# Kernel optimization log

Measured on AMD Instinct MI355X. Metric: run time of the kernel, lower is better.

The kernel has to match this reference:

```python
import math
import jax, jax.numpy as jnp
import numpy as np

B, N, D = 16, 2304, 1024
H = W = 1344
M = 8
HV = WV = 48  # h_vis = h_patches//2; N == HV*WV
N_RAYS, N_SAMPLES = 24, 20
K_STEEP, THETA = 50.0, 0.3


def setup_inputs() -> dict:
    key = jax.random.key(0)
    ks = jax.random.split(key, 6)
    visual_tokens = jax.random.normal(ks[0], (B, N, D), jnp.float32)
    depth_map = jax.random.uniform(ks[1], (B, H, W), jnp.float32) * 10.0
    masks = jax.random.randint(ks[2], (M, H, W), 0, 2).astype(jnp.int32)
    rgb_gate_w = jax.random.normal(ks[3], (D,), jnp.float32) / math.sqrt(D)
    depth_w = jax.random.normal(ks[4], (28, D), jnp.float32) / math.sqrt(28.0)
    depth_b = jnp.zeros((D,), jnp.float32)
    ln_gamma = jnp.ones((D,), jnp.float32)
    ln_beta = jnp.zeros((D,), jnp.float32)
    return dict(visual_tokens=visual_tokens, depth_map=depth_map, masks=masks,
                rgb_gate_w=rgb_gate_w, depth_w=depth_w, depth_b=depth_b,
                ln_gamma=ln_gamma, ln_beta=ln_beta, h_vis=HV, w_vis=WV)


def _bilinear_border(img, x, y):
    # img [B,H,W]; x,y [P] pixel coords; F.grid_sample bilinear, border pad, align_corners=True
    Hh, Ww = img.shape[-2], img.shape[-1]
    x = jnp.clip(x, 0.0, Ww - 1.0)
    y = jnp.clip(y, 0.0, Hh - 1.0)
    x0 = jnp.floor(x); y0 = jnp.floor(y)
    wx = x - x0; wy = y - y0
    x0i = x0.astype(jnp.int32); y0i = y0.astype(jnp.int32)
    x1i = jnp.minimum(x0i + 1, Ww - 1); y1i = jnp.minimum(y0i + 1, Hh - 1)
    v00 = img[:, y0i, x0i]; v01 = img[:, y0i, x1i]
    v10 = img[:, y1i, x0i]; v11 = img[:, y1i, x1i]
    return v00 * (1 - wx) * (1 - wy) + v01 * wx * (1 - wy) + v10 * (1 - wx) * wy + v11 * wx * wy


def _bilinear_zeros(img, x, y):
    # img [H,W]; F.grid_sample bilinear, zeros pad, align_corners=True
    Hh, Ww = img.shape
    x0 = jnp.floor(x); y0 = jnp.floor(y)
    wx = x - x0; wy = y - y0
    x0i = x0.astype(jnp.int32); y0i = y0.astype(jnp.int32)
    x1i = x0i + 1; y1i = y0i + 1

    def tap(yy, xx, w):
        valid = (xx >= 0) & (xx < Ww) & (yy >= 0) & (yy < Hh)
        v = img[jnp.clip(yy, 0, Hh - 1), jnp.clip(xx, 0, Ww - 1)]
        return jnp.where(valid, v * w, 0.0)

    return (tap(y0i, x0i, (1 - wx) * (1 - wy)) + tap(y0i, x1i, wx * (1 - wy)) +
            tap(y1i, x0i, (1 - wx) * wy) + tap(y1i, x1i, wx * wy))


def _forward(visual_tokens, depth_map, masks, rgb_gate_w, depth_w, depth_b, ln_gamma, ln_beta, h_vis, w_vis):
    Bn, Hh, Ww = depth_map.shape
    ph, pw = Hh // h_vis, Ww // w_vis  # adaptive_avg_pool2d divides evenly -> block mean
    angles = jnp.linspace(0.0, 2.0 * math.pi, N_RAYS + 1)[:-1]
    cos_a, sin_a = jnp.cos(angles), jnp.sin(angles)
    max_r = min(Hh, Ww) * 0.45
    t_vals = jnp.linspace(0.0, max_r, N_SAMPLES)

    def per_mask(binm_i):
        binm = binm_i.astype(jnp.float32)  # [H,W] binary (RLE-decoded in torch)
        coverage = binm.reshape(h_vis, ph, w_vis, pw).mean(axis=(1, 3))  # [hv,wv]
        soft2d = jax.nn.sigmoid(K_STEEP * (coverage - THETA))
        # --- DB-style soft gated attention pool over N tokens ---
        log_soft = jnp.log(jnp.clip(soft2d.reshape(-1), 1e-8))
        scores = jnp.einsum('bnd,d->bn', visual_tokens, rgb_gate_w)
        weights = jax.nn.softmax(scores + log_soft[None, :], axis=-1)
        rgb = jnp.einsum('bn,bnd->bd', weights, visual_tokens)
        # --- masked depth stats (mean, unbiased std) ---
        count = binm.sum()
        mean_d = jnp.einsum('bhw,hw->b', depth_map, binm) / jnp.maximum(count, 1.0)
        sq = jnp.einsum('bhw,hw->b', depth_map * depth_map, binm)
        var = (sq - count * mean_d * mean_d) / jnp.maximum(count - 1.0, 1.0)
        std_d = jnp.sqrt(jnp.clip(jnp.where(count > 1.0, var, 0.0), 0.0))
        # --- soft centroid (normalized to ~[0,1]) ---
        soft_sum = soft2d.sum() + 1e-8
        cx = (soft2d.sum(0) * jnp.arange(w_vis, dtype=jnp.float32)).sum() / (soft_sum * w_vis)
        cy = (soft2d.sum(1) * jnp.arange(h_vis, dtype=jnp.float32)).sum() / (soft_sum * h_vis)
        # --- 24-ray radial depth profile ---
        cx_pix = cx * (Ww - 1); cy_pix = cy * (Hh - 1)
        xs_pix = cx_pix + cos_a[:, None] * t_vals[None, :]  # [rays,samples]
        ys_pix = cy_pix + sin_a[:, None] * t_vals[None, :]
        d_samp = _bilinear_border(depth_map, xs_pix.ravel(), ys_pix.ravel()).reshape(Bn, N_RAYS, N_SAMPLES)
        xs_p = xs_pix / (Ww - 1) * (w_vis - 1)
        ys_p = ys_pix / (Hh - 1) * (h_vis - 1)
        sw = _bilinear_zeros(soft2d, xs_p.ravel(), ys_p.ravel()).reshape(N_RAYS, N_SAMPLES)
        sw = jnp.clip(sw, 1e-6)
        w_norm = sw / sw.sum(axis=1, keepdims=True)
        profile = (d_samp * w_norm[None]).sum(-1)  # [B,rays]
        stats = jnp.concatenate([mean_d[:, None], std_d[:, None],
                                 jnp.broadcast_to(cx, (Bn, 1)), jnp.broadcast_to(cy, (Bn, 1)),
                                 profile], axis=1)  # [B,28]
        stats = jnp.where(count > 0.0, stats, 0.0)  # empty-mask fallback
        # --- depth_proj: Linear(28->D) + LayerNorm ---
        h = stats @ depth_w + depth_b
        mu = h.mean(-1, keepdims=True)
        v = ((h - mu) ** 2).mean(-1, keepdims=True)
        dep = (h - mu) / jnp.sqrt(v + 1e-5) * ln_gamma + ln_beta
        return rgb, dep

    return jax.vmap(per_mask)(masks)  # ([M,B,D], [M,B,D])


def reference(visual_tokens, depth_map, masks, rgb_gate_w, depth_w, depth_b, ln_gamma, ln_beta, h_vis, w_vis):
    return _forward(visual_tokens, depth_map, masks, rgb_gate_w, depth_w, depth_b,
                    ln_gamma, ln_beta, int(h_vis), int(w_vis))
```

## Files before the change

### kernel.cpp

```cpp
#include <hip/hip_runtime.h>
#include <math.h>

constexpr int BN   = 16;
constexpr int NTOK = 2304;
constexpr int DDIM = 1024;
constexpr int HH   = 1344;
constexpr int WWp  = 1344;
constexpr int HWPIX = HH * WWp;
constexpr int NM   = 8;
constexpr int HVIS = 48;
constexpr int PATCH = 28;
constexpr int NRAY = 24;
constexpr int NSMP = 20;
constexpr int NPROB = HVIS * HVIS;

__global__ void k_pack(const int* __restrict__ masks, uchar4* __restrict__ packed,
                       float* __restrict__ cnt, float* __restrict__ sumd,
                       float* __restrict__ sumd2) {
    int i = blockIdx.x * blockDim.x + threadIdx.x;
    if (blockIdx.x == 0) {
        int t = threadIdx.x;
        if (t < 8) cnt[t] = 0.f;
        else if (t < 136) sumd[t - 8] = 0.f;
        else if (t < 264) sumd2[t - 136] = 0.f;
    }
    unsigned b0 = 0, b1 = 0, b2 = 0, b3 = 0;
#pragma unroll
    for (int m = 0; m < 8; m++) {
        int4 mv = ((const int4*)(masks + (size_t)m * HWPIX))[i];
        b0 |= (unsigned)(mv.x & 1) << m;
        b1 |= (unsigned)(mv.y & 1) << m;
        b2 |= (unsigned)(mv.z & 1) << m;
        b3 |= (unsigned)(mv.w & 1) << m;
    }
    packed[i] = make_uchar4((unsigned char)b0, (unsigned char)b1,
                            (unsigned char)b2, (unsigned char)b3);
}

__global__ void k_cov(const unsigned char* __restrict__ packed,
                      float* __restrict__ cov, float* __restrict__ cnt) {
    int patch = blockIdx.x;
    int pi = patch / HVIS, pj = patch - pi * HVIS;
    int t = threadIdx.x;
    float c[8] = {0, 0, 0, 0, 0, 0, 0, 0};
    for (int p = t; p < PATCH * PATCH; p += 256) {
        int r = p / PATCH, q = p - r * PATCH;
        unsigned pb = packed[(pi * PATCH + r) * WWp + pj * PATCH + q];
#pragma unroll
        for (int m = 0; m < 8; m++) c[m] += (float)((pb >> m) & 1u);
    }
    __shared__ float red[8][256];
#pragma unroll
    for (int m = 0; m < 8; m++) red[m][t] = c[m];
    __syncthreads();
    for (int o = 128; o; o >>= 1) {
        if (t < o) {
#pragma unroll
            for (int m = 0; m < 8; m++) red[m][t] += red[m][t + o];
        }
        __syncthreads();
    }
    if (t < 8) {
        cov[t * NPROB + patch] = red[t][0];
        atomicAdd(&cnt[t], red[t][0]);
    }
}

__global__ void k_scores(const float* __restrict__ tokens,
                         const float* __restrict__ gate,
                         float* __restrict__ scores) {
    int row = blockIdx.x * 4 + (threadIdx.x >> 6);
    int lane = threadIdx.x & 63;
    const float4* tp = (const float4*)(tokens + (size_t)row * DDIM);
    const float4* gp = (const float4*)gate;
    float s = 0.f;
#pragma unroll
    for (int i = 0; i < 4; i++) {
        int idx = lane + i * 64;
        float4 tv = tp[idx];
        float4 gv = gp[idx];
        s += tv.x * gv.x + tv.y * gv.y + tv.z * gv.z + tv.w * gv.w;
    }
#pragma unroll
    for (int o = 32; o; o >>= 1) s += __shfl_down(s, o, 64);
    if (lane == 0) scores[row] = s;
}

__global__ void k_soft(const float* __restrict__ cov, float* __restrict__ soft,
                       float* __restrict__ lsoft, float* __restrict__ cent) {
    int m = blockIdx.x, t = threadIdx.x;
    float psum = 0.f, psx = 0.f, psy = 0.f;
#pragma unroll
    for (int i = 0; i < 9; i++) {
        int n = t + i * 256;
        float c = cov[m * NPROB + n] * (1.0f / 784.0f);
        float s = 1.0f / (1.0f + expf(-50.0f * (c - 0.3f)));
        soft[m * NPROB + n] = s;
        lsoft[m * NPROB + n] = logf(fmaxf(s, 1e-8f));
        int row = n / HVIS, col = n - row * HVIS;
        psum += s;
        psx += s * (float)col;
        psy += s * (float)row;
    }
    __shared__ float r0[256], r1[256], r2[256];
    r0[t] = psum; r1[t] = psx; r2[t] = psy;
    __syncthreads();
    for (int o = 128; o; o >>= 1) {
        if (t < o) { r0[t] += r0[t + o]; r1[t] += r1[t + o]; r2[t] += r2[t + o]; }
        __syncthreads();
    }
    if (t == 0) {
        float ss = r0[0] + 1e-8f;
        float cx = r1[0] / (ss * (float)HVIS);
        float cy = r2[0] / (ss * (float)HVIS);
        cent[m * 4 + 0] = cx;
        cent[m * 4 + 1] = cy;
        cent[m * 4 + 2] = cx * (float)(WWp - 1);
        cent[m * 4 + 3] = cy * (float)(HH - 1);
    }
}

constexpr int KPT = 7;
__global__ void k_depthstats(const float* __restrict__ depth,
                             const uchar4* __restrict__ packed,
                             float* __restrict__ sumd, float* __restrict__ sumd2) {
    int b = blockIdx.y;
    int t = threadIdx.x;
    int base4 = blockIdx.x * (256 * KPT);
    const float4* dp4 = (const float4*)(depth + (size_t)b * HWPIX);

    float4 dv[KPT];
    uchar4 pv[KPT];
#pragma unroll
    for (int k = 0; k < KPT; k++) {
        int idx = base4 + k * 256 + t;
        dv[k] = dp4[idx];
        pv[k] = packed[idx];
    }

    float acc[8] = {0, 0, 0, 0, 0, 0, 0, 0};
    float acc2[8] = {0, 0, 0, 0, 0, 0, 0, 0};
#pragma unroll
    for (int k = 0; k < KPT; k++) {
        float dd[4] = {dv[k].x, dv[k].y, dv[k].z, dv[k].w};
        unsigned bb[4] = {pv[k].x, pv[k].y, pv[k].z, pv[k].w};
#pragma unroll
        for (int j = 0; j < 4; j++) {
            float d = dd[j];
            float sq = d * d;
            unsigned byte = bb[j];
#pragma unroll
            for (int m = 0; m < 8; m++) {
                float f = (float)((byte >> m) & 1u);
                acc[m] = fmaf(f, d, acc[m]);
                acc2[m] = fmaf(f, sq, acc2[m]);
            }
        }
    }
#pragma unroll
    for (int o = 32; o; o >>= 1) {
#pragma unroll
        for (int m = 0; m < 8; m++) {
            acc[m] += __shfl_down(acc[m], o, 64);
            acc2[m] += __shfl_down(acc2[m], o, 64);
        }
    }
    __shared__ float red[2][8][4];
    int wid = threadIdx.x >> 6, lane = threadIdx.x & 63;
    if (lane == 0) {
#pragma unroll
        for (int m = 0; m < 8; m++) {
            red[0][m][wid] = acc[m];
            red[1][m][wid] = acc2[m];
        }
    }
    __syncthreads();
    if (threadIdx.x < 16) {
        int s = threadIdx.x >> 3, m = threadIdx.x & 7;
        float v = red[s][m][0] + red[s][m][1] + red[s][m][2] + red[s][m][3];
        atomicAdd((s ? sumd2 : sumd) + m * BN + b, v);
    }
}

__global__ void k_rays(const float* __restrict__ depth, const float* __restrict__ soft,
                       const float* __restrict__ cent, float* __restrict__ prof) {
    int m = blockIdx.x, b = blockIdx.y, t = threadIdx.x;
    __shared__ float s_sw[NRAY * NSMP], s_d[NRAY * NSMP];
    float cxp = cent[m * 4 + 2], cyp = cent[m * 4 + 3];
    if (t < NRAY * NSMP) {
        int r = t / NSMP, s = t - r * NSMP;
        float ang = (float)r * (6.28318530717958647692f / (float)NRAY);
        float tv = (float)s * (604.8f / (float)(NSMP - 1));
        float xs = fmaf(cosf(ang), tv, cxp);
        float ys = fmaf(sinf(ang), tv, cyp);
        float x = fminf(fmaxf(xs, 0.0f), (float)(WWp - 1));
        float y = fminf(fmaxf(ys, 0.0f), (float)(HH - 1));
        float x0f = floorf(x), y0f = floorf(y);
        float wx = x - x0f, wy = y - y0f;
        int x0 = (int)x0f, y0 = (int)y0f;
        int x1 = min(x0 + 1, WWp - 1), y1 = min(y0 + 1, HH - 1);
        const float* dpb = depth + (size_t)b * HWPIX;
        float v00 = dpb[y0 * WWp + x0], v01 = dpb[y0 * WWp + x1];
        float v10 = dpb[y1 * WWp + x0], v11 = dpb[y1 * WWp + x1];
        float ds = v00 * (1 - wx) * (1 - wy) + v01 * wx * (1 - wy) +
                   v10 * (1 - wx) * wy + v11 * wx * wy;
        const float* sp = soft + m * NPROB;
        float xp = xs * ((float)(HVIS - 1) / (float)(WWp - 1));
        float yp = ys * ((float)(HVIS - 1) / (float)(HH - 1));
        float xp0 = floorf(xp), yp0 = floorf(yp);
        float ux = xp - xp0, uy = yp - yp0;
        int a0 = (int)xp0, c0 = (int)yp0;
        float sw = 0.f;
        int xx[2] = {a0, a0 + 1};
        int yy[2] = {c0, c0 + 1};
        float wxt[2] = {1.0f - ux, ux};
        float wyt[2] = {1.0f - uy, uy};
#pragma unroll
        for (int ii = 0; ii < 2; ii++) {
#pragma unroll
            for (int jj = 0; jj < 2; jj++) {
                int yv = yy[ii], xv = xx[jj];
                bool valid = (xv >= 0) && (xv < HVIS) && (yv >= 0) && (yv < HVIS);
                float vv = sp[min(max(yv, 0), HVIS - 1) * HVIS + min(max(xv, 0), HVIS - 1)];
                sw += valid ? vv * wyt[ii] * wxt[jj] : 0.0f;
            }
        }
        sw = fmaxf(sw, 1e-6f);
        s_sw[t] = sw;
        s_d[t] = ds;
    }
    __syncthreads();
    if (t < NRAY) {
        float wsum = 0.f, dot = 0.f;
#pragma unroll
        for (int s = 0; s < NSMP; s++) {
            float w = s_sw[t * NSMP + s];
            wsum += w;
            dot += s_d[t * NSMP + s] * w;
        }
        prof[(m * BN + b) * NRAY + t] = dot / wsum;
    }
}

__global__ void k_wred(const float* __restrict__ scores, const float* __restrict__ lsoft,
                       float* __restrict__ smax, float* __restrict__ ssum) {
    int mb = blockIdx.x;
    int m = mb >> 4, b = mb & 15;
    int t = threadIdx.x;
    float v[9];
    float pm = -1e30f;
#pragma unroll
    for (int i = 0; i < 9; i++) {
        int n = t + i * 256;
        float x = scores[b * NTOK + n] + lsoft[m * NTOK + n];
        v[i] = x;
        pm = fmaxf(pm, x);
    }
    __shared__ float r[256];
    r[t] = pm;
    __syncthreads();
    for (int o = 128; o; o >>= 1) {
        if (t < o) r[t] = fmaxf(r[t], r[t + o]);
        __syncthreads();
    }
    float mx = r[0];
    __syncthreads();
    float ps = 0.f;
#pragma unroll
    for (int i = 0; i < 9; i++) ps += expf(v[i] - mx);
    r[t] = ps;
    __syncthreads();
    for (int o = 128; o; o >>= 1) {
        if (t < o) r[t] += r[t + o];
        __syncthreads();
    }
    if (t == 0) { smax[mb] = mx; ssum[mb] = r[0]; }
}

__global__ void k_rgb(const float* __restrict__ tokens, const float* __restrict__ scores,
                      const float* __restrict__ lsoft, const float* __restrict__ smax,
                      const float* __restrict__ ssum, float* __restrict__ rgb) {
    constexpr int CHUNK = 72;
    int b = blockIdx.x, chunk = blockIdx.y, t = threadIdx.x;
    int n0 = chunk * CHUNK;
    __shared__ float wl[8][CHUNK];
    for (int i = t; i < 8 * CHUNK; i += 256) {
        int m = i / CHUNK, k = i - m * CHUNK;
        int n = n0 + k;
        wl[m][k] = expf(scores[b * NTOK + n] + lsoft[m * NTOK + n] - smax[m * BN + b]) /
                   ssum[m * BN + b];
    }
    __syncthreads();
    float acc[8][4] = {};
    const float4* tp = (const float4*)(tokens + ((size_t)(b * NTOK + n0)) * DDIM);
#pragma unroll 8
    for (int k = 0; k < CHUNK; k++) {
        float4 tok = tp[(size_t)k * 256 + t];
#pragma unroll
        for (int m = 0; m < 8; m++) {
            float w = wl[m][k];
            acc[m][0] = fmaf(w, tok.x, acc[m][0]);
            acc[m][1] = fmaf(w, tok.y, acc[m][1]);
            acc[m][2] = fmaf(w, tok.z, acc[m][2]);
            acc[m][3] = fmaf(w, tok.w, acc[m][3]);
        }
    }
    int d0 = t * 4;
#pragma unroll
    for (int m = 0; m < 8; m++) {
#pragma unroll
        for (int j = 0; j < 4; j++)
            atomicAdd(&rgb[((size_t)(m * BN + b)) * DDIM + d0 + j], acc[m][j]);
    }
}

__global__ void k_dep(const float* __restrict__ sumd, const float* __restrict__ sumd2,
                      const float* __restrict__ cnt, const float* __restrict__ cent,
                      const float* __restrict__ prof, const float* __restrict__ dw,
                      const float* __restrict__ db, const float* __restrict__ gamma,
                      const float* __restrict__ beta, float* __restrict__ dep) {
    int m = blockIdx.x, b = blockIdx.y, t = threadIdx.x;
    __shared__ float st[28];
    float c = cnt[m];
    if (t < 28) {
        float v;
        if (t == 0) {
            v = sumd[m * BN + b] / fmaxf(c, 1.0f);
        } else if (t == 1) {
            float mean = sumd[m * BN + b] / fmaxf(c, 1.0f);
            float var = (sumd2[m * BN + b] - c * mean * mean) / fmaxf(c - 1.0f, 1.0f);
            var = (c > 1.0f) ? var : 0.0f;
            v = sqrtf(fmaxf(var, 0.0f));
        } else if (t == 2) v = cent[m * 4 + 0];
        else if (t == 3) v = cent[m * 4 + 1];
        else v = prof[(m * BN + b) * NRAY + (t - 4)];
        st[t] = (c > 0.0f) ? v : 0.0f;
    }
    __syncthreads();
    int d0 = t * 4;
    float4 hb = *(const float4*)(db + d0);
    float h0 = hb.x, h1 = hb.y, h2 = hb.z, h3 = hb.w;
#pragma unroll
    for (int k = 0; k < 28; k++) {
        float s = st[k];
        float4 w = *(const float4*)(dw + k * DDIM + d0);
        h0 = fmaf(s, w.x, h0);
        h1 = fmaf(s, w.y, h1);
        h2 = fmaf(s, w.z, h2);
        h3 = fmaf(s, w.w, h3);
    }
    float ps = h0 + h1 + h2 + h3;
    float pq = h0 * h0 + h1 * h1 + h2 * h2 + h3 * h3;
    __shared__ float rs[256], rq[256];
    rs[t] = ps; rq[t] = pq;
    __syncthreads();
    for (int o = 128; o; o >>= 1) {
        if (t < o) { rs[t] += rs[t + o]; rq[t] += rq[t + o]; }
        __syncthreads();
    }
    float mu = rs[0] * (1.0f / (float)DDIM);
    float var = rq[0] * (1.0f / (float)DDIM) - mu * mu;
    float inv = 1.0f / sqrtf(var + 1e-5f);
    float4 g = *(const float4*)(gamma + d0);
    float4 be = *(const float4*)(beta + d0);
    size_t o = ((size_t)(m * BN + b)) * DDIM + d0;
    dep[o + 0] = (h0 - mu) * inv * g.x + be.x;
    dep[o + 1] = (h1 - mu) * inv * g.y + be.y;
    dep[o + 2] = (h2 - mu) * inv * g.z + be.z;
    dep[o + 3] = (h3 - mu) * inv * g.w + be.w;
}

extern "C" void kernel_launch(void* const* d_in, const int* in_sizes, int n_in,
                              void* d_out, int out_size, void* d_ws, size_t ws_size,
                              hipStream_t stream) {
    const float* tokens = (const float*)d_in[0];
    const float* depth  = (const float*)d_in[1];
    const int*   masks  = (const int*)d_in[2];
    const float* gate   = (const float*)d_in[3];
    const float* dw     = (const float*)d_in[4];
    const float* db     = (const float*)d_in[5];
    const float* gamma  = (const float*)d_in[6];
    const float* beta   = (const float*)d_in[7];
    float* out = (float*)d_out;

    char* ws = (char*)d_ws;
    size_t off = 0;
    auto alloc = [&](size_t bytes) {
        size_t o = off;
        off = (off + bytes + 255) & ~(size_t)255;
        return o;
    };
    unsigned char* packed = (unsigned char*)(ws + alloc(HWPIX));
    float* cov    = (float*)(ws + alloc((size_t)NM * NPROB * 4));
    float* cnt    = (float*)(ws + alloc(NM * 4));
    float* soft   = (float*)(ws + alloc((size_t)NM * NPROB * 4));
    float* lsoft  = (float*)(ws + alloc((size_t)NM * NPROB * 4));
    float* cent   = (float*)(ws + alloc(NM * 4 * 4));
    float* sumd   = (float*)(ws + alloc(NM * BN * 4));
    float* sumd2  = (float*)(ws + alloc(NM * BN * 4));
    float* scores = (float*)(ws + alloc((size_t)BN * NTOK * 4));
    float* smax   = (float*)(ws + alloc(NM * BN * 4));
    float* ssum   = (float*)(ws + alloc(NM * BN * 4));
    float* prof   = (float*)(ws + alloc((size_t)NM * BN * NRAY * 4));

    hipMemsetAsync(out, 0, (size_t)NM * BN * DDIM * 4, stream);

    k_pack<<<HWPIX / 4 / 256, 256, 0, stream>>>(masks, (uchar4*)packed,
                                                cnt, sumd, sumd2);
    k_cov<<<NPROB, 256, 0, stream>>>(packed, cov, cnt);
    k_scores<<<BN * NTOK / 4, 256, 0, stream>>>(tokens, gate, scores);
    k_soft<<<NM, 256, 0, stream>>>(cov, soft, lsoft, cent);
    k_depthstats<<<dim3(HWPIX / 4 / (256 * KPT), BN), 256, 0, stream>>>(
        depth, (const uchar4*)packed, sumd, sumd2);
    k_rays<<<dim3(NM, BN), 512, 0, stream>>>(depth, soft, cent, prof);
    k_wred<<<NM * BN, 256, 0, stream>>>(scores, lsoft, smax, ssum);
    k_rgb<<<dim3(BN, NTOK / 72), 256, 0, stream>>>(tokens, scores, lsoft, smax, ssum, out);
    k_dep<<<dim3(NM, BN), 256, 0, stream>>>(sumd, sumd2, cnt, cent, prof, dw, db,
                                            gamma, beta,
                                            out + (size_t)NM * BN * DDIM);
}
```

Measured before the change: 543.1 us.

## Batch global loads ahead of compute with sched barriers and launch bounds

Several kernels (mask packing, score dot products, depth statistics, rgb pooling) now issue all their global loads up front into registers. A scheduling barrier separates those loads from the arithmetic so more memory requests are in flight at once. Launch bounds are added, depth-stats work per thread drops from 7 to 4, and the rgb weight tile in shared memory is transposed so the 8 per-mask weights come from two vector reads. The risk is higher register pressure, and the barriers stop the compiler from interleaving loads and math on its own.

After: 621.0 us. 1.14x slower.

```diff
diff --git a/kernel.cpp b/kernel.cpp
--- a/kernel.cpp
+++ b/kernel.cpp
@@ -14,9 +14,10 @@
 constexpr int NSMP = 20;
 constexpr int NPROB = HVIS * HVIS;
 
-__global__ void k_pack(const int* __restrict__ masks, uchar4* __restrict__ packed,
-                       float* __restrict__ cnt, float* __restrict__ sumd,
-                       float* __restrict__ sumd2) {
+__global__ __launch_bounds__(256, 4) void k_pack(
+        const int* __restrict__ masks, uchar4* __restrict__ packed,
+        float* __restrict__ cnt, float* __restrict__ sumd,
+        float* __restrict__ sumd2) {
     int i = blockIdx.x * blockDim.x + threadIdx.x;
     if (blockIdx.x == 0) {
         int t = threadIdx.x;
@@ -24,14 +25,18 @@
         else if (t < 136) sumd[t - 8] = 0.f;
         else if (t < 264) sumd2[t - 136] = 0.f;
     }
+    int4 mv[8];
+#pragma unroll
+    for (int m = 0; m < 8; m++)
+        mv[m] = ((const int4*)(masks + (size_t)m * HWPIX))[i];
+    __builtin_amdgcn_sched_barrier(0);
     unsigned b0 = 0, b1 = 0, b2 = 0, b3 = 0;
 #pragma unroll
     for (int m = 0; m < 8; m++) {
-        int4 mv = ((const int4*)(masks + (size_t)m * HWPIX))[i];
-        b0 |= (unsigned)(mv.x & 1) << m;
-        b1 |= (unsigned)(mv.y & 1) << m;
-        b2 |= (unsigned)(mv.z & 1) << m;
-        b3 |= (unsigned)(mv.w & 1) << m;
+        b0 |= (unsigned)(mv[m].x & 1) << m;
+        b1 |= (unsigned)(mv[m].y & 1) << m;
+        b2 |= (unsigned)(mv[m].z & 1) << m;
+        b3 |= (unsigned)(mv[m].w & 1) << m;
     }
     packed[i] = make_uchar4((unsigned char)b0, (unsigned char)b1,
                             (unsigned char)b2, (unsigned char)b3);
@@ -66,21 +71,25 @@
     }
 }
 
-__global__ void k_scores(const float* __restrict__ tokens,
-                         const float* __restrict__ gate,
-                         float* __restrict__ scores) {
+__global__ __launch_bounds__(256, 4) void k_scores(
+        const float* __restrict__ tokens, const float* __restrict__ gate,
+        float* __restrict__ scores) {
     int row = blockIdx.x * 4 + (threadIdx.x >> 6);
     int lane = threadIdx.x & 63;
     const float4* tp = (const float4*)(tokens + (size_t)row * DDIM);
     const float4* gp = (const float4*)gate;
+    float4 tv[4], gv[4];
+#pragma unroll
+    for (int i = 0; i < 4; i++) {
+        tv[i] = tp[lane + i * 64];
+        gv[i] = gp[lane + i * 64];
+    }
+    __builtin_amdgcn_sched_barrier(0);
     float s = 0.f;
 #pragma unroll
-    for (int i = 0; i < 4; i++) {
-        int idx = lane + i * 64;
-        float4 tv = tp[idx];
-        float4 gv = gp[idx];
-        s += tv.x * gv.x + tv.y * gv.y + tv.z * gv.z + tv.w * gv.w;
-    }
+    for (int i = 0; i < 4; i++)
+        s += tv[i].x * gv[i].x + tv[i].y * gv[i].y +
+             tv[i].z * gv[i].z + tv[i].w * gv[i].w;
 #pragma unroll
     for (int o = 32; o; o >>= 1) s += __shfl_down(s, o, 64);
     if (lane == 0) scores[row] = s;
@@ -120,10 +129,10 @@
     }
 }
 
-constexpr int KPT = 7;
-__global__ void k_depthstats(const float* __restrict__ depth,
-                             const uchar4* __restrict__ packed,
-                             float* __restrict__ sumd, float* __restrict__ sumd2) {
+constexpr int KPT = 4;
+__global__ __launch_bounds__(256, 4) void k_depthstats(
+        const float* __restrict__ depth, const uchar4* __restrict__ packed,
+        float* __restrict__ sumd, float* __restrict__ sumd2) {
     int b = blockIdx.y;
     int t = threadIdx.x;
     int base4 = blockIdx.x * (256 * KPT);
@@ -137,6 +146,7 @@
         dv[k] = dp4[idx];
         pv[k] = packed[idx];
     }
+    __builtin_amdgcn_sched_barrier(0);
 
     float acc[8] = {0, 0, 0, 0, 0, 0, 0, 0};
     float acc2[8] = {0, 0, 0, 0, 0, 0, 0, 0};
@@ -277,32 +287,43 @@
     if (t == 0) { smax[mb] = mx; ssum[mb] = r[0]; }
 }
 
-__global__ void k_rgb(const float* __restrict__ tokens, const float* __restrict__ scores,
-                      const float* __restrict__ lsoft, const float* __restrict__ smax,
-                      const float* __restrict__ ssum, float* __restrict__ rgb) {
+__global__ __launch_bounds__(256, 2) void k_rgb(
+        const float* __restrict__ tokens, const float* __restrict__ scores,
+        const float* __restrict__ lsoft, const float* __restrict__ smax,
+        const float* __restrict__ ssum, float* __restrict__ rgb) {
     constexpr int CHUNK = 72;
     int b = blockIdx.x, chunk = blockIdx.y, t = threadIdx.x;
     int n0 = chunk * CHUNK;
-    __shared__ float wl[8][CHUNK];
-    for (int i = t; i < 8 * CHUNK; i += 256) {
-        int m = i / CHUNK, k = i - m * CHUNK;
+    __shared__ float wl[CHUNK][8];
+    for (int i = t; i < CHUNK * 8; i += 256) {
+        int k = i >> 3, m = i & 7;
         int n = n0 + k;
-        wl[m][k] = expf(scores[b * NTOK + n] + lsoft[m * NTOK + n] - smax[m * BN + b]) /
+        wl[k][m] = expf(scores[b * NTOK + n] + lsoft[m * NTOK + n] - smax[m * BN + b]) /
                    ssum[m * BN + b];
     }
     __syncthreads();
     float acc[8][4] = {};
     const float4* tp = (const float4*)(tokens + ((size_t)(b * NTOK + n0)) * DDIM);
-#pragma unroll 8
-    for (int k = 0; k < CHUNK; k++) {
-        float4 tok = tp[(size_t)k * 256 + t];
-#pragma unroll
-        for (int m = 0; m < 8; m++) {
-            float w = wl[m][k];
-            acc[m][0] = fmaf(w, tok.x, acc[m][0]);
-            acc[m][1] = fmaf(w, tok.y, acc[m][1]);
-            acc[m][2] = fmaf(w, tok.z, acc[m][2]);
-            acc[m][3] = fmaf(w, tok.w, acc[m][3]);
+    for (int c = 0; c < CHUNK / 8; c++) {
+        float4 tk[8];
+#pragma unroll
+        for (int j = 0; j < 8; j++)
+            tk[j] = tp[(size_t)(c * 8 + j) * 256 + t];
+        __builtin_amdgcn_sched_barrier(0);
+#pragma unroll
+        for (int j = 0; j < 8; j++) {
+            int k = c * 8 + j;
+            const float4* wp = (const float4*)&wl[k][0];
+            float4 w0 = wp[0], w1 = wp[1];
+            float wm[8] = {w0.x, w0.y, w0.z, w0.w, w1.x, w1.y, w1.z, w1.w};
+#pragma unroll
+            for (int m = 0; m < 8; m++) {
+                float w = wm[m];
+                acc[m][0] = fmaf(w, tk[j].x, acc[m][0]);
+                acc[m][1] = fmaf(w, tk[j].y, acc[m][1]);
+                acc[m][2] = fmaf(w, tk[j].z, acc[m][2]);
+                acc[m][3] = fmaf(w, tk[j].w, acc[m][3]);
+            }
         }
     }
     int d0 = t * 4;
```
